# Performance work log

Measured on AMD Instinct MI355X. Metric: run time of the kernel, lower is better.

## Reference

```python
import math
import jax, jax.numpy as jnp
import numpy as np

_GELU_C = math.sqrt(2.0 / math.pi)

def _gelu_tanh(x):
    return 0.5 * x * (1.0 + jnp.tanh(_GELU_C * (x + 0.044715 * x * x * x)))

def _l2_normalize(v, eps=1e-12):
    # matches F.normalize: v / max(||v||, eps)
    n = jnp.sqrt(jnp.sum(v * v, axis=-1, keepdims=True))
    return v / jnp.maximum(n, eps)

def setup_inputs() -> dict:
    key = jax.random.key(0)
    k1, k2, k3 = jax.random.split(key, 3)
    B, T, D = 8, 2048, 1024
    x = jax.random.normal(k1, (B, T, D), dtype=jnp.float32)
    # nn.Parameter initial values from the module
    log_alpha = jnp.asarray(math.log(math.exp(0.5) - 1.0), dtype=jnp.float32)
    log_sigma = jnp.asarray(math.log(1.0), dtype=jnp.float32)
    return {"x": x, "log_alpha": log_alpha, "log_sigma": log_sigma}

def reference(x, log_alpha, log_sigma):
    B, T, D = x.shape
    alpha = jax.nn.softplus(log_alpha)
    sigma = jax.nn.softplus(log_sigma)
    scale = 1.0 / math.sqrt(D)
    # full strictly-past causal attention (triu with diagonal=0 masks self too)
    sim = jnp.einsum('btd,bsd->bts', x, x) * scale            # [B,T,T]
    causal = jnp.triu(jnp.ones((T, T), dtype=bool), k=0)      # True = masked
    sim = jnp.where(causal[None], -jnp.inf, sim)
    # NaN-safe masked softmax: fully-masked rows (t=0) -> all zeros,
    # matching torch softmax + nan_to_num(nan=0.0)
    m = jnp.max(sim, axis=-1, keepdims=True)
    m_safe = jnp.where(jnp.isfinite(m), m, 0.0)
    e = jnp.exp(sim - m_safe)                                 # -inf -> 0
    denom = jnp.sum(e, axis=-1, keepdims=True)
    attn = jnp.where(denom > 0, e / jnp.where(denom > 0, denom, 1.0), 0.0)
    context = jnp.einsum('bts,bsd->btd', attn, x)             # [B,T,D]
    cos_sim = jnp.sum(_l2_normalize(x) * _l2_normalize(context), axis=-1)  # [B,T]
    novelty = jnp.clip(1.0 - cos_sim, 0.0, 2.0) / 2.0
    novelty = jnp.nan_to_num(novelty, nan=1.0)
    gate = 1.0 + alpha * jnp.tanh(sigma * novelty[..., None])
    return _gelu_tanh(x * gate)
```

## Files before the change

### kernel.cpp

```cpp
#include <hip/hip_runtime.h>
#include <math.h>

#define TN 2048
#define DN 1024
#define NEG_INF (-3.0e38f)

typedef __attribute__((ext_vector_type(8))) _Float16 half8;
typedef __attribute__((ext_vector_type(4))) _Float16 half4v;
typedef __attribute__((ext_vector_type(4))) float f32x4;

__device__ __forceinline__ f32x4 mfma16(half8 a, half8 b, f32x4 c) {
  return __builtin_amdgcn_mfma_f32_16x16x32_f16(a, b, c, 0, 0, 0);
}

__device__ __forceinline__ int img_off(int key, int f) {
  const int kg = key >> 2;
  const int p  = ((kg & 1) << 2) | (kg >> 1);
  return (f >> 4) * 512 + p * 64 + (key & 3) * 16 + (f & 15);
}

__global__ __launch_bounds__(256) void convert_x(const float* __restrict__ x,
                                                 _Float16* __restrict__ w) {
  const long long gid = (long long)blockIdx.x * 256 + threadIdx.x;
  const long long e   = gid * 8;
  const int bt   = (int)(e >> 15);
  const int et   = (int)(e & 32767);
  const int f16b = et >> 9;
  const int p    = (et >> 6) & 7;
  const int row  = (et >> 4) & 3;
  const int col0 = et & 15;
  const int kg   = ((p & 3) << 1) | (p >> 2);
  const int key  = kg * 4 + row;
  const size_t xoff = ((size_t)bt * 32 + key) * DN + f16b * 16 + col0;
  float4 u0 = *(const float4*)(x + xoff);
  float4 u1 = *(const float4*)(x + xoff + 4);
  half8 h = {(_Float16)u0.x, (_Float16)u0.y, (_Float16)u0.z, (_Float16)u0.w,
             (_Float16)u1.x, (_Float16)u1.y, (_Float16)u1.z, (_Float16)u1.w};
  *(half8*)(w + e) = h;
}

template <bool WS>
__global__ __launch_bounds__(512, 2)
void attn_gate(const float* __restrict__ x, const _Float16* __restrict__ wsx,
               const float* __restrict__ pla, const float* __restrict__ pls,
               float* __restrict__ out) {
  __shared__ _Float16 Kbuf[2][32768];
  __shared__ float Sred[2][32][33];
  __shared__ _Float16 Pq[32][40];
  __shared__ float m_s[32], l_s[32], corr_s[32], gate_s[32];

  const int tid = threadIdx.x;
  const int w   = tid >> 6;
  const int l   = tid & 63;
  const int lr  = l & 15;
  const int lg  = l >> 4;
  const int ti  = w & 1;
  const int tj  = (w >> 1) & 1;
  const int kq  = w >> 2;

  const int b  = blockIdx.x & 7;
  const int pr = blockIdx.x >> 3;

  const float alpha = log1pf(expf(pla[0]));
  const float sigma = log1pf(expf(pls[0]));

  const float* xb = x + (size_t)b * TN * DN;
  float*       ob = out + (size_t)b * TN * DN;

  for (int hv = 0; hv < 2; ++hv) {
    const int qt    = hv ? (63 - pr) : pr;
    const int qbase = qt * 32;
    const int nkt   = qt + 1;

    if constexpr (WS) {
      const _Float16* t0 = wsx + (size_t)(b * 64 + 0) * 32768;
#pragma unroll
      for (int i = 0; i < 8; ++i)
        __builtin_amdgcn_global_load_lds(
            (const __attribute__((address_space(1))) void*)(t0 + w * 4096 + i * 512 + l * 8),
            (__attribute__((address_space(3))) void*)(&Kbuf[0][w * 4096 + i * 512]), 16, 0, 0);
      if (nkt > 1) {
        const _Float16* t1 = wsx + (size_t)(b * 64 + 1) * 32768;
#pragma unroll
        for (int i = 0; i < 8; ++i)
          __builtin_amdgcn_global_load_lds(
              (const __attribute__((address_space(1))) void*)(t1 + w * 4096 + i * 512 + l * 8),
              (__attribute__((address_space(3))) void*)(&Kbuf[1][w * 4096 + i * 512]), 16, 0, 0);
      }
    } else {
      const int skey = tid >> 4, sc = tid & 15;
      for (int t = 0; t < (nkt > 1 ? 2 : 1); ++t) {
        const float* kp = xb + (size_t)(t * 32 + skey) * DN + sc * 4;
#pragma unroll
        for (int j = 0; j < 16; ++j) {
          const int f = sc * 4 + 64 * j;
          float4 v = *(const float4*)(kp + 64 * j);
          half4v h = {(_Float16)v.x, (_Float16)v.y, (_Float16)v.z, (_Float16)v.w};
          *(half4v*)&Kbuf[t][img_off(skey, f)] = h;
        }
      }
    }

    half8 qf[16];
    if constexpr (WS) {
      const _Float16* qtile = wsx + (size_t)(b * 64 + qt) * 32768;
      const int qrow = ti * 16 + lr;
      const int qkg  = qrow >> 2;
      const int qp   = (((qkg & 1) << 2) | (qkg >> 1)) * 64 + (qrow & 3) * 16 + (lg & 1) * 8;
#pragma unroll
      for (int s = 0; s < 16; ++s)
        qf[s] = *(const half8*)&qtile[(kq * 32 + s * 2 + (lg >> 1)) * 512 + qp];
    } else {
      const float* qp = xb + (size_t)(qbase + ti * 16 + lr) * DN + kq * 512 + lg * 8;
#pragma unroll
      for (int s = 0; s < 16; ++s) {
        float4 a = ((const float4*)(qp + s * 32))[0];
        float4 c = ((const float4*)(qp + s * 32))[1];
        half8 h;
        h[0]=(_Float16)a.x; h[1]=(_Float16)a.y; h[2]=(_Float16)a.z; h[3]=(_Float16)a.w;
        h[4]=(_Float16)c.x; h[5]=(_Float16)c.y; h[6]=(_Float16)c.z; h[7]=(_Float16)c.w;
        qf[s] = h;
      }
    }

    f32x4 oacc[2][8];
#pragma unroll
    for (int rt = 0; rt < 2; ++rt)
#pragma unroll
      for (int ct = 0; ct < 8; ++ct)
        oacc[rt][ct] = f32x4{0.f, 0.f, 0.f, 0.f};

    if (tid < 32) { m_s[tid] = NEG_INF; l_s[tid] = 0.0f; }
    __syncthreads();

    for (int kt = 0; kt < nkt; ++kt) {
      const int cur = kt & 1;

      {
        f32x4 sacc = f32x4{0.f, 0.f, 0.f, 0.f};
        const int kg  = tj * 4 + (lr >> 2);
        const int kgp = ((kg & 1) << 2) | (kg >> 1);
        const int bk  = kgp * 64 + (lr & 3) * 16 + (lg & 1) * 8;
        const _Float16* kb = &Kbuf[cur][0];
#pragma unroll
        for (int s = 0; s < 16; ++s) {
          half8 bf = *(const half8*)&kb[(kq * 32 + s * 2 + (lg >> 1)) * 512 + bk];
          sacc = mfma16(qf[s], bf, sacc);
        }
#pragma unroll
        for (int j = 0; j < 4; ++j)
          Sred[kq][ti * 16 + lg * 4 + j][tj * 16 + lr] = sacc[j];
      }
      __syncthreads();

      {
        const int r   = tid >> 4;
        const int c0  = tid & 15;
        const int qg  = qbase + r;
        const int kb0 = kt * 32;
        float s0 = (Sred[0][r][c0]      + Sred[1][r][c0])      * 0.03125f;
        float s1 = (Sred[0][r][c0 + 16] + Sred[1][r][c0 + 16]) * 0.03125f;
        const bool v0 = (kb0 + c0)      < qg;
        const bool v1 = (kb0 + c0 + 16) < qg;
        if (!v0) s0 = NEG_INF;
        if (!v1) s1 = NEG_INF;
        float tmax = fmaxf(s0, s1);
#pragma unroll
        for (int d = 1; d < 16; d <<= 1) tmax = fmaxf(tmax, __shfl_xor(tmax, d));
        const float m_old = m_s[r];
        const float m_new = fmaxf(m_old, tmax);
        float p0 = v0 ? __expf(s0 - m_new) : 0.0f;
        float p1 = v1 ? __expf(s1 - m_new) : 0.0f;
        float ps = p0 + p1;
#pragma unroll
        for (int d = 1; d < 16; d <<= 1) ps += __shfl_xor(ps, d);
        const float corr = (m_old > 0.5f * NEG_INF) ? __expf(m_old - m_new) : 0.0f;
        if (c0 == 0) {
          m_s[r]    = m_new;
          l_s[r]    = l_s[r] * corr + ps;
          corr_s[r] = corr;
        }
        Pq[r][c0]      = (_Float16)p0;
        Pq[r][c0 + 16] = (_Float16)p1;
      }
      __syncthreads();

      {
#pragma unroll
        for (int rt = 0; rt < 2; ++rt)
#pragma unroll
          for (int j = 0; j < 4; ++j) {
            const float cr = corr_s[rt * 16 + lg * 4 + j];
#pragma unroll
            for (int ct = 0; ct < 8; ++ct) oacc[rt][ct][j] *= cr;
          }
        half8 a0 = *(const half8*)&Pq[lr][lg * 8];
        half8 a1 = *(const half8*)&Pq[16 + lr][lg * 8];
        half4v lo[8], hi[8];
        const uint32_t ab =
            (uint32_t)(uintptr_t)(void*)&Kbuf[cur][w * 4096 + l * 4];
#define TRRD(CT, O0, O1)                                                      \
        asm volatile("ds_read_b64_tr_b16 %0, %2 offset:" O0 "\n\t"            \
                     "ds_read_b64_tr_b16 %1, %2 offset:" O1                   \
                     : "=v"(lo[CT]), "=v"(hi[CT]) : "v"(ab));
        TRRD(0, "0",    "512")  TRRD(1, "1024", "1536")
        TRRD(2, "2048", "2560") TRRD(3, "3072", "3584")
        TRRD(4, "4096", "4608") TRRD(5, "5120", "5632")
        TRRD(6, "6144", "6656") TRRD(7, "7168", "7680")
#undef TRRD
        asm volatile("s_waitcnt lgkmcnt(0)" ::: "memory");
        __builtin_amdgcn_sched_barrier(0);
#pragma unroll
        for (int ct = 0; ct < 8; ++ct) {
          half8 bf = __builtin_shufflevector(lo[ct], hi[ct], 0, 1, 2, 3, 4, 5, 6, 7);
          oacc[0][ct] = mfma16(a0, bf, oacc[0][ct]);
          oacc[1][ct] = mfma16(a1, bf, oacc[1][ct]);
        }
      }
      __syncthreads();

      if (kt + 2 < nkt) {
        if constexpr (WS) {
          const _Float16* tn = wsx + (size_t)(b * 64 + kt + 2) * 32768;
#pragma unroll
          for (int i = 0; i < 8; ++i)
            __builtin_amdgcn_global_load_lds(
                (const __attribute__((address_space(1))) void*)(tn + w * 4096 + i * 512 + l * 8),
                (__attribute__((address_space(3))) void*)(&Kbuf[cur][w * 4096 + i * 512]), 16, 0, 0);
        } else {
          const int skey = tid >> 4, sc = tid & 15;
          const float* kp = xb + (size_t)((kt + 2) * 32 + skey) * DN + sc * 4;
#pragma unroll
          for (int j = 0; j < 16; ++j) {
            const int f = sc * 4 + 64 * j;
            float4 v = *(const float4*)(kp + 64 * j);
            half4v h = {(_Float16)v.x, (_Float16)v.y, (_Float16)v.z, (_Float16)v.w};
            *(half4v*)&Kbuf[cur][img_off(skey, f)] = h;
          }
        }
      }
    }

    {
      float* ered = &Sred[0][0][0];
#pragma unroll
      for (int rt = 0; rt < 2; ++rt)
#pragma unroll
        for (int j = 0; j < 4; ++j) {
          const int row = rt * 16 + lg * 4 + j;
          const float* xr = xb + (size_t)(qbase + row) * DN + w * 128 + lr;
          float a1 = 0.f, a2 = 0.f, a3 = 0.f;
#pragma unroll
          for (int ct = 0; ct < 8; ++ct) {
            const float xv = xr[ct * 16];
            const float ov = oacc[rt][ct][j];
            a1 += xv * ov; a2 += xv * xv; a3 += ov * ov;
          }
#pragma unroll
          for (int d = 1; d < 16; d <<= 1) {
            a1 += __shfl_xor(a1, d);
            a2 += __shfl_xor(a2, d);
            a3 += __shfl_xor(a3, d);
          }
          if (lr == 0) {
            float* e = ered + (row * 8 + w) * 4;
            e[0] = a1; e[1] = a2; e[2] = a3;
          }
        }
    }
    __syncthreads();
    if (tid < 32) {
      const float* ered = &Sred[0][0][0];
      float SxO = 0.f, Sxx = 0.f, SOO = 0.f;
#pragma unroll
      for (int wv = 0; wv < 8; ++wv) {
        const float* e = ered + (tid * 8 + wv) * 4;
        SxO += e[0]; Sxx += e[1]; SOO += e[2];
      }
      const float lden = l_s[tid];
      float cosv = 0.0f;
      if (lden > 0.0f) {
        const float nx = fmaxf(sqrtf(Sxx), 1e-12f);
        const float nc = fmaxf(sqrtf(SOO) / lden, 1e-12f);
        cosv = (SxO / lden) / (nx * nc);
      }
      float nov = fminf(fmaxf(1.0f - cosv, 0.0f), 2.0f) * 0.5f;
      gate_s[tid] = 1.0f + alpha * tanhf(sigma * nov);
    }
    __syncthreads();
    {
#pragma unroll
      for (int rt = 0; rt < 2; ++rt)
#pragma unroll
        for (int j = 0; j < 4; ++j) {
          const int row = rt * 16 + lg * 4 + j;
          const float g = gate_s[row];
          const float* xr = xb + (size_t)(qbase + row) * DN + w * 128 + lr;
          float* orow     = ob + (size_t)(qbase + row) * DN + w * 128 + lr;
#pragma unroll
          for (int ct = 0; ct < 8; ++ct) {
            const float z = xr[ct * 16] * g;
            const float u = 0.7978845608028654f * (z + 0.044715f * z * z * z);
            orow[ct * 16] = 0.5f * z * (1.0f + tanhf(u));
          }
        }
    }
    __syncthreads();
  }
}

extern "C" void kernel_launch(void* const* d_in, const int* in_sizes, int n_in,
                              void* d_out, int out_size, void* d_ws, size_t ws_size,
                              hipStream_t stream) {
  const float* x  = (const float*)d_in[0];
  const float* la = (const float*)d_in[1];
  const float* ls = (const float*)d_in[2];
  float* out = (float*)d_out;
  const size_t need = (size_t)8 * 64 * 32768 * 2;
  if (ws_size >= need) {
    convert_x<<<dim3(8192), dim3(256), 0, stream>>>(x, (_Float16*)d_ws);
    attn_gate<true><<<dim3(256), dim3(512), 0, stream>>>(
        x, (const _Float16*)d_ws, la, ls, out);
  } else {
    attn_gate<false><<<dim3(256), dim3(512), 0, stream>>>(
        x, (const _Float16*)nullptr, la, ls, out);
  }
}
```

Before: 220.7 us.

## Repartition QK^T across warps into 4-way K-split with two key tiles

Reassigns the eight warps so each handles one 16-row query tile and a quarter of the feature dimension, computing both 16-key column tiles per warp. Halving the per-warp Q fragments cuts register use, and the launch bound drops the min-blocks hint. Partial scores are now reduced from four Sred slices instead of two, and __syncthreads is replaced by a custom lgkmcnt wait plus s_barrier. The trade is more LDS traffic in the reduction and possibly lower occupancy, and the custom barrier skips any vmcnt wait, which is risky if global-to-LDS loads are in flight.

```diff
diff --git a/kernel.cpp b/kernel.cpp
--- a/kernel.cpp
+++ b/kernel.cpp
@@ -12,6 +12,8 @@
 __device__ __forceinline__ f32x4 mfma16(half8 a, half8 b, f32x4 c) {
   return __builtin_amdgcn_mfma_f32_16x16x32_f16(a, b, c, 0, 0, 0);
 }
+
+#define BAR_LDS() asm volatile("s_waitcnt lgkmcnt(0)\ns_barrier" ::: "memory")
 
 __device__ __forceinline__ int img_off(int key, int f) {
   const int kg = key >> 2;
@@ -40,12 +42,12 @@
 }
 
 template <bool WS>
-__global__ __launch_bounds__(512, 2)
+__global__ __launch_bounds__(512)
 void attn_gate(const float* __restrict__ x, const _Float16* __restrict__ wsx,
                const float* __restrict__ pla, const float* __restrict__ pls,
                float* __restrict__ out) {
   __shared__ _Float16 Kbuf[2][32768];
-  __shared__ float Sred[2][32][33];
+  __shared__ float Sred[4][32][34];
   __shared__ _Float16 Pq[32][40];
   __shared__ float m_s[32], l_s[32], corr_s[32], gate_s[32];
 
@@ -54,9 +56,8 @@
   const int l   = tid & 63;
   const int lr  = l & 15;
   const int lg  = l >> 4;
-  const int ti  = w & 1;
-  const int tj  = (w >> 1) & 1;
-  const int kq  = w >> 2;
+  const int kq  = w & 3;
+  const int ti  = w >> 2;
 
   const int b  = blockIdx.x & 7;
   const int pr = blockIdx.x >> 3;
@@ -101,19 +102,19 @@
       }
     }
 
-    half8 qf[16];
+    half8 qf[8];
     if constexpr (WS) {
       const _Float16* qtile = wsx + (size_t)(b * 64 + qt) * 32768;
       const int qrow = ti * 16 + lr;
       const int qkg  = qrow >> 2;
       const int qp   = (((qkg & 1) << 2) | (qkg >> 1)) * 64 + (qrow & 3) * 16 + (lg & 1) * 8;
 #pragma unroll
-      for (int s = 0; s < 16; ++s)
-        qf[s] = *(const half8*)&qtile[(kq * 32 + s * 2 + (lg >> 1)) * 512 + qp];
+      for (int s = 0; s < 8; ++s)
+        qf[s] = *(const half8*)&qtile[(kq * 16 + s * 2 + (lg >> 1)) * 512 + qp];
     } else {
-      const float* qp = xb + (size_t)(qbase + ti * 16 + lr) * DN + kq * 512 + lg * 8;
-#pragma unroll
-      for (int s = 0; s < 16; ++s) {
+      const float* qp = xb + (size_t)(qbase + ti * 16 + lr) * DN + kq * 256 + lg * 8;
+#pragma unroll
+      for (int s = 0; s < 8; ++s) {
         float4 a = ((const float4*)(qp + s * 32))[0];
         float4 c = ((const float4*)(qp + s * 32))[1];
         half8 h;
@@ -133,33 +134,43 @@
     if (tid < 32) { m_s[tid] = NEG_INF; l_s[tid] = 0.0f; }
     __syncthreads();
 
+    const int kg0  = lr >> 2;
+    const int bk0  = ((((kg0 & 1) << 2) | (kg0 >> 1)) << 6) + (lr & 3) * 16 + (lg & 1) * 8;
+    const int kg1  = 4 + (lr >> 2);
+    const int bk1  = ((((kg1 & 1) << 2) | (kg1 >> 1)) << 6) + (lr & 3) * 16 + (lg & 1) * 8;
+
     for (int kt = 0; kt < nkt; ++kt) {
       const int cur = kt & 1;
 
       {
-        f32x4 sacc = f32x4{0.f, 0.f, 0.f, 0.f};
-        const int kg  = tj * 4 + (lr >> 2);
-        const int kgp = ((kg & 1) << 2) | (kg >> 1);
-        const int bk  = kgp * 64 + (lr & 3) * 16 + (lg & 1) * 8;
+        f32x4 s0 = f32x4{0.f, 0.f, 0.f, 0.f};
+        f32x4 s1 = f32x4{0.f, 0.f, 0.f, 0.f};
         const _Float16* kb = &Kbuf[cur][0];
 #pragma unroll
-        for (int s = 0; s < 16; ++s) {
-          half8 bf = *(const half8*)&kb[(kq * 32 + s * 2 + (lg >> 1)) * 512 + bk];
-          sacc = mfma16(qf[s], bf, sacc);
-        }
-#pragma unroll
-        for (int j = 0; j < 4; ++j)
-          Sred[kq][ti * 16 + lg * 4 + j][tj * 16 + lr] = sacc[j];
-      }
-      __syncthreads();
+        for (int s = 0; s < 8; ++s) {
+          const int base = (kq * 16 + s * 2 + (lg >> 1)) * 512;
+          half8 bf0 = *(const half8*)&kb[base + bk0];
+          half8 bf1 = *(const half8*)&kb[base + bk1];
+          s0 = mfma16(qf[s], bf0, s0);
+          s1 = mfma16(qf[s], bf1, s1);
+        }
+#pragma unroll
+        for (int j = 0; j < 4; ++j) {
+          Sred[kq][ti * 16 + lg * 4 + j][lr]      = s0[j];
+          Sred[kq][ti * 16 + lg * 4 + j][16 + lr] = s1[j];
+        }
+      }
+      BAR_LDS();
 
       {
         const int r   = tid >> 4;
         const int c0  = tid & 15;
         const int qg  = qbase + r;
         const int kb0 = kt * 32;
-        float s0 = (Sred[0][r][c0]      + Sred[1][r][c0])      * 0.03125f;
-        float s1 = (Sred[0][r][c0 + 16] + Sred[1][r][c0 + 16]) * 0.03125f;
+        float s0 = (Sred[0][r][c0] + Sred[1][r][c0] +
+                    Sred[2][r][c0] + Sred[3][r][c0]) * 0.03125f;
+        float s1 = (Sred[0][r][c0 + 16] + Sred[1][r][c0 + 16] +
+                    Sred[2][r][c0 + 16] + Sred[3][r][c0 + 16]) * 0.03125f;
         const bool v0 = (kb0 + c0)      < qg;
         const bool v1 = (kb0 + c0 + 16) < qg;
         if (!v0) s0 = NEG_INF;
@@ -183,7 +194,7 @@
         Pq[r][c0]      = (_Float16)p0;
         Pq[r][c0 + 16] = (_Float16)p1;
       }
-      __syncthreads();
+      BAR_LDS();
 
       {
 #pragma unroll
```

Result: faster. 196.5 us (-11.0%).
